# Kernel tuning notes

Hardware: AMD Instinct MI355X
Metric: run time of the kernel (lower is better)

The kernel has to match this reference:

```python
import jax, jax.numpy as jnp
import numpy as np

L_COMPUTE = 32   # topological levels after primary inputs
W = 32768        # gates per level
K = 4            # max fan-in (distinct pins 1..K per gate)
B = 128          # parallel test patterns
T = 16           # number of cell types in the library
N = (L_COMPUTE + 1) * W


def setup_inputs() -> dict:
    key = jax.random.key(0)
    k1, k2, k3, k4 = jax.random.split(key, 4)
    # binary logic values per node per pattern (only level-0 rows are real inputs;
    # the rest are overwritten by propagation, matching g.ndata['h'] = feature)
    feature = jax.random.bernoulli(k1, 0.5, (N, B)).astype(jnp.float32)
    # truth table: activation[cell_type, input_combination] in {0,1}
    activation = jax.random.bernoulli(k2, 0.5, (T, 2 ** K)).astype(jnp.float32)
    # each gate in level l draws its K inputs from level l-1
    src_idx = jax.random.randint(k3, (L_COMPUTE, W, K), 0, W).astype(jnp.int32)
    cell_type = jax.random.randint(k4, (L_COMPUTE, W), 0, T).astype(jnp.int32)
    # edge pin numbers: distinct pins 1..K per gate (edges.data['x'])
    pins = jnp.broadcast_to(jnp.arange(1, K + 1, dtype=jnp.int32), (L_COMPUTE, W, K))
    pins = jnp.asarray(pins)
    return {"feature": feature, "activation": activation, "src_idx": src_idx,
            "cell_type": cell_type, "pins": pins}


def reference(feature, activation, src_idx, cell_type, pins):
    Wn = src_idx.shape[1]
    Bn = feature.shape[1]
    h0 = feature[:Wn]  # primary-input level keeps its feature values

    def step(h, xs):
        src, ctype, pin = xs          # [W,K], [W], [W,K]
        hs = h[src]                   # gather: [W,K,B]
        # gcn_msg: m = 2^(x-1) * h_src ; gcn_reduce: sum over incoming edges
        w = jnp.exp2(pin.astype(h.dtype) - 1.0)          # [W,K]
        m = jnp.einsum('wk,wkb->wb', w, hs)              # [W,B] encoded input combo
        # NodeApplyModule: truth-table lookup activation[cell_type, h]
        h_new = activation[ctype[:, None], m.astype(jnp.int32)]  # [W,B]
        return h_new, h_new

    _, ys = jax.lax.scan(step, h0, (src_idx, cell_type, pins))
    # g.ndata.pop('h'): values for ALL nodes, level 0 unchanged
    return jnp.concatenate([h0, ys.reshape(-1, Bn)], axis=0)
```

## Files before the change

kernel.cpp:

```cpp
#include <hip/hip_runtime.h>
#include <stdint.h>

typedef uint32_t u32;
typedef unsigned long long u64;
typedef float f4 __attribute__((ext_vector_type(4)));

#define WGATES 32768
#define BATCH  128
#define LAYERS 32
#define NTYPES 16
#define NC 512
#define WPL (WGATES * 4)
#define F4L (WGATES * BATCH / 4)

#define WS_SUB_OFF    1024
#define WS_LVL2_OFF   34816
#define WS_DONE_OFF   35840
#define WS_S_OFF      69632
#define WS_NEED_BYTES ((size_t)(WS_S_OFF + 33 * WPL) * 4)

__device__ __forceinline__ u32 agent_load(const u32* p) {
    return __hip_atomic_load(p, __ATOMIC_RELAXED, __HIP_MEMORY_SCOPE_AGENT);
}
__device__ __forceinline__ void agent_store(u32* p, u32 v) {
    __hip_atomic_store(p, v, __ATOMIC_RELAXED, __HIP_MEMORY_SCOPE_AGENT);
}
__device__ __forceinline__ u32 agent_add(u32* p, u32 v) {
    return __hip_atomic_fetch_add(p, v, __ATOMIC_RELAXED, __HIP_MEMORY_SCOPE_AGENT);
}

__device__ __forceinline__ u32 lut_eval(u32 tt, u32 a, u32 b, u32 c, u32 d) {
    u32 m[16];
    #pragma unroll
    for (int j = 0; j < 16; ++j)
        m[j] = (u32)(((int)(tt << (31 - j))) >> 31);
    u32 na = ~a, nb = ~b, nc = ~c, nd = ~d;
    u32 v0 = (m[1]&a)|(m[0]&na),  v1 = (m[3]&a)|(m[2]&na);
    u32 v2 = (m[5]&a)|(m[4]&na),  v3 = (m[7]&a)|(m[6]&na);
    u32 v4 = (m[9]&a)|(m[8]&na),  v5 = (m[11]&a)|(m[10]&na);
    u32 v6 = (m[13]&a)|(m[12]&na),v7 = (m[15]&a)|(m[14]&na);
    u32 u0 = (b&v1)|(nb&v0), u1 = (b&v3)|(nb&v2);
    u32 u2 = (b&v5)|(nb&v4), u3 = (b&v7)|(nb&v6);
    u32 w0 = (c&u1)|(nc&u0), w1 = (c&u3)|(nc&u2);
    return (d&w1)|(nd&w0);
}

__device__ __forceinline__ void wait_done(const u32* ws, int l, int line, int tid) {
    if (tid == 0) {
        const u32* p = ws + WS_DONE_OFF + (size_t)l * 1024 + line * 16;
        while (agent_load(p) == 0)
            __builtin_amdgcn_s_sleep(4);
    }
    __syncthreads();
    asm volatile("" ::: "memory");
}

__global__ void pack_main(const float* __restrict__ feature,
                          const float* __restrict__ activation,
                          u32* __restrict__ ws) {
    int t = blockIdx.x * 256 + threadIdx.x;
    if (blockIdx.x == 0 && threadIdx.x < NTYPES) {
        u32 tt = 0;
        #pragma unroll
        for (int m = 0; m < 16; ++m)
            tt |= (activation[threadIdx.x * 16 + m] != 0.0f ? 1u : 0u) << m;
        ws[threadIdx.x] = tt;
    }
    int z = (int)blockIdx.x - 1;
    if (z >= 0 && z < 268)
        ws[1024 + z * 256 + threadIdx.x] = 0;
    float v = feature[t];
    u64 m = __ballot(v != 0.0f);
    if ((t & 63) == 0)
        ((u64*)(ws + WS_S_OFF))[t >> 6] = m;
}

__global__ __launch_bounds__(256) void coop_kernel(
        const int* __restrict__ src_idx,
        const int* __restrict__ cell_type,
        u32* __restrict__ ws,
        float* __restrict__ out,
        int NU)
{
    u32* Sb = ws + WS_S_OFF;
    int tid = threadIdx.x;
    __shared__ u32 stt[NTYPES];
    if (tid < NTYPES) stt[tid] = ws[tid];
    __syncthreads();

    if ((int)blockIdx.x < NC) {
        int gid = blockIdx.x * 256 + tid;
        int g = gid >> 2, q = gid & 3;
        int sub = blockIdx.x & 63;
        for (int l = 1; l <= LAYERS; ++l) {
            const int4 s = ((const int4*)(src_idx + (size_t)(l - 1) * WGATES * 4))[g];
            u32 ttv = stt[cell_type[(size_t)(l - 1) * WGATES + g]];
            if (l > 1) wait_done(ws, l - 1, sub, tid);
            const u32* Sp = Sb + (size_t)(l - 1) * WPL;
            u32 a = Sp[(u32)s.x * 4 + q];
            u32 b = Sp[(u32)s.y * 4 + q];
            u32 c = Sp[(u32)s.z * 4 + q];
            u32 d = Sp[(u32)s.w * 4 + q];
            agent_store(Sb + (size_t)l * WPL + gid, lut_eval(ttv, a, b, c, d));
            asm volatile("s_waitcnt vmcnt(0)" ::: "memory");
            __syncthreads();
            if (tid == 0) {
                u32* subp = ws + WS_SUB_OFF + (size_t)l * 1024 + sub * 16;
                u32 old = agent_add(subp, 1u);
                if (old == (u32)(NC / 64 - 1)) {
                    u32 old2 = agent_add(ws + WS_LVL2_OFF + (size_t)l * 16, 1u);
                    if (old2 == 63u) {
                        u32* donep = ws + WS_DONE_OFF + (size_t)l * 1024;
                        #pragma unroll
                        for (int j = 0; j < 64; ++j)
                            agent_store(donep + j * 16, 1u);
                    }
                }
            }
        }
    } else {
        int ub = blockIdx.x - NC;
        for (int l = 0; l <= LAYERS; ++l) {
            if (l >= 1) wait_done(ws, l, ub & 63, tid);
            const u32* Sl = Sb + (size_t)l * WPL;
            f4* ob = (f4*)(out + (size_t)l * WGATES * BATCH);
            for (u32 i = (u32)ub * 256u + tid; i < (u32)F4L; i += (u32)NU * 256u) {
                u32 wb = Sl[i >> 3];
                u32 sh = (i & 7) * 4;
                f4 f;
                f.x = ((wb >> (sh    )) & 1) ? 1.0f : 0.0f;
                f.y = ((wb >> (sh + 1)) & 1) ? 1.0f : 0.0f;
                f.z = ((wb >> (sh + 2)) & 1) ? 1.0f : 0.0f;
                f.w = ((wb >> (sh + 3)) & 1) ? 1.0f : 0.0f;
                __builtin_nontemporal_store(f, ob + i);
            }
        }
    }
}

__global__ void pack_kernel_fb(const float* __restrict__ feature,
                               const float* __restrict__ activation,
                               float* __restrict__ out,
                               u32* __restrict__ tt_ws,
                               u32* __restrict__ buf0) {
    int t = blockIdx.x * 256 + threadIdx.x;
    if (blockIdx.x == 0 && threadIdx.x < NTYPES) {
        u32 tt = 0;
        #pragma unroll
        for (int m = 0; m < 16; ++m)
            tt |= (activation[threadIdx.x * 16 + m] != 0.0f ? 1u : 0u) << m;
        tt_ws[threadIdx.x] = tt;
    }
    float v = feature[t];
    out[t] = v;
    u64 m = __ballot(v != 0.0f);
    if ((t & 63) == 0)
        ((u64*)buf0)[t >> 6] = m;
}

__global__ void fused_kernel_fb(const u32* __restrict__ prev,
                                u32* __restrict__ next,
                                const int* __restrict__ src_idx,
                                const int* __restrict__ cell_type,
                                const u32* __restrict__ tt_ws,
                                const u32* __restrict__ upacked,
                                float* __restrict__ uout,
                                int do_compute)
{
    int tid = threadIdx.x;
    if (do_compute && blockIdx.x < 512) {
        int gl = tid >> 2, q = tid & 3;
        int wg = blockIdx.x * 64 + gl;
        const int4 s = ((const int4*)src_idx)[wg];
        u32 tt = tt_ws[cell_type[wg]];
        u32 a = prev[(size_t)s.x * 4 + q];
        u32 b = prev[(size_t)s.y * 4 + q];
        u32 c = prev[(size_t)s.z * 4 + q];
        u32 d = prev[(size_t)s.w * 4 + q];
        next[(size_t)wg * 4 + q] = lut_eval(tt, a, b, c, d);
        return;
    }
    if (uout == nullptr) return;
    int ub = do_compute ? (int)blockIdx.x - 512 : (int)blockIdx.x;
    #pragma unroll
    for (int r = 0; r < 2; ++r) {
        int fi = ((ub * 2 + r) * 256 + tid) * 4;
        u32 wb = upacked[fi >> 5];
        int sh = fi & 31;
        f4 f;
        f.x = ((wb >> (sh    )) & 1) ? 1.0f : 0.0f;
        f.y = ((wb >> (sh + 1)) & 1) ? 1.0f : 0.0f;
        f.z = ((wb >> (sh + 2)) & 1) ? 1.0f : 0.0f;
        f.w = ((wb >> (sh + 3)) & 1) ? 1.0f : 0.0f;
        ((f4*)uout)[fi >> 2] = f;
    }
}

static void launch_fallback(const float* feature, const float* activation,
                            const int* src_idx, const int* cell_type,
                            float* out, void* d_ws, hipStream_t stream) {
    u32* tt_ws = (u32*)d_ws;
    u32* bufA = (u32*)((char*)d_ws + 1024);
    u32* bufB = (u32*)((char*)d_ws + 1024 + WGATES * 16);
    pack_kernel_fb<<<WGATES * BATCH / 256, 256, 0, stream>>>(
        feature, activation, out, tt_ws, bufA);
    for (int l = 1; l <= LAYERS; ++l) {
        u32* prev = ((l - 1) & 1) ? bufB : bufA;
        u32* next = ((l - 1) & 1) ? bufA : bufB;
        float* uout = (l >= 2) ? out + (size_t)(l - 1) * WGATES * BATCH : nullptr;
        fused_kernel_fb<<<512 + 2048, 256, 0, stream>>>(
            prev, next,
            src_idx + (size_t)(l - 1) * WGATES * 4,
            cell_type + (size_t)(l - 1) * WGATES,
            tt_ws, prev, uout, 1);
    }
    u32* s32 = ((LAYERS - 1) & 1) ? bufA : bufB;
    fused_kernel_fb<<<2048, 256, 0, stream>>>(
        s32, s32, src_idx, cell_type, tt_ws,
        s32, out + (size_t)LAYERS * WGATES * BATCH, 0);
}

extern "C" void kernel_launch(void* const* d_in, const int* in_sizes, int n_in,
                              void* d_out, int out_size, void* d_ws, size_t ws_size,
                              hipStream_t stream) {
    const float* feature    = (const float*)d_in[0];
    const float* activation = (const float*)d_in[1];
    const int*   src_idx    = (const int*)d_in[2];
    const int*   cell_type  = (const int*)d_in[3];
    float* out = (float*)d_out;

    bool coop_ok = (ws_size >= WS_NEED_BYTES);
    int G = 0, NU = 0;
    if (coop_ok) {
        int dev = 0;
        (void)hipGetDevice(&dev);
        int numCU = 0, bpc = 0;
        if (hipDeviceGetAttribute(&numCU, hipDeviceAttributeMultiprocessorCount, dev)
                != hipSuccess) coop_ok = false;
        if (coop_ok &&
            hipOccupancyMaxActiveBlocksPerMultiprocessor(
                &bpc, (const void*)coop_kernel, 256, 0) != hipSuccess) coop_ok = false;
        if (coop_ok) {
            G = bpc * numCU;
            if (G > 2048) G = 2048;
            NU = G - NC;
            if (NU < 256) coop_ok = false;
        }
    }

    if (coop_ok) {
        u32* ws = (u32*)d_ws;
        pack_main<<<WGATES * BATCH / 256, 256, 0, stream>>>(feature, activation, ws);
        void* args[] = {(void*)&src_idx, (void*)&cell_type, (void*)&ws,
                        (void*)&out, (void*)&NU};
        hipError_t e = hipLaunchCooperativeKernel(
            (const void*)coop_kernel, dim3(G), dim3(256), args, 0, stream);
        if (e == hipSuccess) return;
    }
    launch_fallback(feature, activation, src_idx, cell_type, out, d_ws, stream);
}
```

Baseline: 168.2 us.

## Use one thread per gate with uint4 gathers and fewer compute blocks

The compute role of the cooperative kernel now uses 128 blocks instead of 512, with one thread per gate instead of four. Each thread gathers all 128 pattern bits of every input with one 16-byte load, builds the truth-table masks once, and runs four mux evaluations. The barrier tree shrinks to 16 sub-groups, and compute waiters spin with a shorter sleep than unpack waiters. Unpack blocks are split into eight contiguous slices of each level for better locality. The aim is to cut per-level synchronisation and gather instruction counts, at the cost of less parallelism on the critical path and freeing CUs for the unpack/store work.

```diff
diff --git a/kernel.cpp b/kernel.cpp
--- a/kernel.cpp
+++ b/kernel.cpp
@@ -9,7 +9,7 @@
 #define BATCH  128
 #define LAYERS 32
 #define NTYPES 16
-#define NC 512
+#define NC 128
 #define WPL (WGATES * 4)
 #define F4L (WGATES * BATCH / 4)
 
@@ -25,15 +25,19 @@
 __device__ __forceinline__ void agent_store(u32* p, u32 v) {
     __hip_atomic_store(p, v, __ATOMIC_RELAXED, __HIP_MEMORY_SCOPE_AGENT);
 }
+__device__ __forceinline__ void agent_store64(u64* p, u64 v) {
+    __hip_atomic_store(p, v, __ATOMIC_RELAXED, __HIP_MEMORY_SCOPE_AGENT);
+}
 __device__ __forceinline__ u32 agent_add(u32* p, u32 v) {
     return __hip_atomic_fetch_add(p, v, __ATOMIC_RELAXED, __HIP_MEMORY_SCOPE_AGENT);
 }
 
-__device__ __forceinline__ u32 lut_eval(u32 tt, u32 a, u32 b, u32 c, u32 d) {
-    u32 m[16];
+__device__ __forceinline__ void lut_masks(u32 tt, u32 m[16]) {
     #pragma unroll
     for (int j = 0; j < 16; ++j)
         m[j] = (u32)(((int)(tt << (31 - j))) >> 31);
+}
+__device__ __forceinline__ u32 lut_mux(const u32 m[16], u32 a, u32 b, u32 c, u32 d) {
     u32 na = ~a, nb = ~b, nc = ~c, nd = ~d;
     u32 v0 = (m[1]&a)|(m[0]&na),  v1 = (m[3]&a)|(m[2]&na);
     u32 v2 = (m[5]&a)|(m[4]&na),  v3 = (m[7]&a)|(m[6]&na);
@@ -45,11 +49,12 @@
     return (d&w1)|(nd&w0);
 }
 
-__device__ __forceinline__ void wait_done(const u32* ws, int l, int line, int tid) {
+__device__ __forceinline__ void wait_done(const u32* ws, int l, int line,
+                                          int tid, int slp) {
     if (tid == 0) {
         const u32* p = ws + WS_DONE_OFF + (size_t)l * 1024 + line * 16;
-        while (agent_load(p) == 0)
-            __builtin_amdgcn_s_sleep(4);
+        if (slp == 1) { while (agent_load(p) == 0) __builtin_amdgcn_s_sleep(1); }
+        else         { while (agent_load(p) == 0) __builtin_amdgcn_s_sleep(8); }
     }
     __syncthreads();
     asm volatile("" ::: "memory");
@@ -89,27 +94,34 @@
     __syncthreads();
 
     if ((int)blockIdx.x < NC) {
-        int gid = blockIdx.x * 256 + tid;
-        int g = gid >> 2, q = gid & 3;
-        int sub = blockIdx.x & 63;
+        int g = blockIdx.x * 256 + tid;
+        int sub = blockIdx.x & 15;
         for (int l = 1; l <= LAYERS; ++l) {
             const int4 s = ((const int4*)(src_idx + (size_t)(l - 1) * WGATES * 4))[g];
             u32 ttv = stt[cell_type[(size_t)(l - 1) * WGATES + g]];
-            if (l > 1) wait_done(ws, l - 1, sub, tid);
-            const u32* Sp = Sb + (size_t)(l - 1) * WPL;
-            u32 a = Sp[(u32)s.x * 4 + q];
-            u32 b = Sp[(u32)s.y * 4 + q];
-            u32 c = Sp[(u32)s.z * 4 + q];
-            u32 d = Sp[(u32)s.w * 4 + q];
-            agent_store(Sb + (size_t)l * WPL + gid, lut_eval(ttv, a, b, c, d));
+            if (l > 1) wait_done(ws, l - 1, sub, tid, 1);
+            const uint4* Sp = (const uint4*)(Sb + (size_t)(l - 1) * WPL);
+            uint4 A = Sp[(u32)s.x];
+            uint4 B = Sp[(u32)s.y];
+            uint4 C = Sp[(u32)s.z];
+            uint4 D = Sp[(u32)s.w];
+            u32 m[16];
+            lut_masks(ttv, m);
+            u32 r0 = lut_mux(m, A.x, B.x, C.x, D.x);
+            u32 r1 = lut_mux(m, A.y, B.y, C.y, D.y);
+            u32 r2 = lut_mux(m, A.z, B.z, C.z, D.z);
+            u32 r3 = lut_mux(m, A.w, B.w, C.w, D.w);
+            u64* dst = (u64*)(Sb + (size_t)l * WPL + (size_t)g * 4);
+            agent_store64(dst,     ((u64)r1 << 32) | r0);
+            agent_store64(dst + 1, ((u64)r3 << 32) | r2);
             asm volatile("s_waitcnt vmcnt(0)" ::: "memory");
             __syncthreads();
             if (tid == 0) {
                 u32* subp = ws + WS_SUB_OFF + (size_t)l * 1024 + sub * 16;
                 u32 old = agent_add(subp, 1u);
-                if (old == (u32)(NC / 64 - 1)) {
+                if (old == (u32)(NC / 16 - 1)) {
                     u32 old2 = agent_add(ws + WS_LVL2_OFF + (size_t)l * 16, 1u);
-                    if (old2 == 63u) {
+                    if (old2 == 15u) {
                         u32* donep = ws + WS_DONE_OFF + (size_t)l * 1024;
                         #pragma unroll
                         for (int j = 0; j < 64; ++j)
@@ -120,19 +132,38 @@
         }
     } else {
         int ub = blockIdx.x - NC;
+        bool sliced = (NU & 7) == 0;
+        int x = ub & 7;
+        u32 per = (u32)(NU >> 3);
         for (int l = 0; l <= LAYERS; ++l) {
-            if (l >= 1) wait_done(ws, l, ub & 63, tid);
+            if (l >= 1) wait_done(ws, l, ub & 63, tid, 8);
             const u32* Sl = Sb + (size_t)l * WPL;
             f4* ob = (f4*)(out + (size_t)l * WGATES * BATCH);
-            for (u32 i = (u32)ub * 256u + tid; i < (u32)F4L; i += (u32)NU * 256u) {
-                u32 wb = Sl[i >> 3];
-                u32 sh = (i & 7) * 4;
-                f4 f;
-                f.x = ((wb >> (sh    )) & 1) ? 1.0f : 0.0f;
-                f.y = ((wb >> (sh + 1)) & 1) ? 1.0f : 0.0f;
-                f.z = ((wb >> (sh + 2)) & 1) ? 1.0f : 0.0f;
-                f.w = ((wb >> (sh + 3)) & 1) ? 1.0f : 0.0f;
-                __builtin_nontemporal_store(f, ob + i);
+            if (sliced) {
+                u32 sbeg = (u32)x * (F4L / 8), send = sbeg + F4L / 8;
+                for (u32 i = sbeg + (u32)(ub >> 3) * 256u + tid; i < send;
+                     i += per * 256u) {
+                    u32 wb = Sl[i >> 3];
+                    u32 sh = (i & 7) * 4;
+                    f4 f;
+                    f.x = ((wb >> (sh    )) & 1) ? 1.0f : 0.0f;
+                    f.y = ((wb >> (sh + 1)) & 1) ? 1.0f : 0.0f;
+                    f.z = ((wb >> (sh + 2)) & 1) ? 1.0f : 0.0f;
+                    f.w = ((wb >> (sh + 3)) & 1) ? 1.0f : 0.0f;
+                    __builtin_nontemporal_store(f, ob + i);
+                }
+            } else {
+                for (u32 i = (u32)ub * 256u + tid; i < (u32)F4L;
+                     i += (u32)NU * 256u) {
+                    u32 wb = Sl[i >> 3];
+                    u32 sh = (i & 7) * 4;
+                    f4 f;
+                    f.x = ((wb >> (sh    )) & 1) ? 1.0f : 0.0f;
+                    f.y = ((wb >> (sh + 1)) & 1) ? 1.0f : 0.0f;
+                    f.z = ((wb >> (sh + 2)) & 1) ? 1.0f : 0.0f;
+                    f.w = ((wb >> (sh + 3)) & 1) ? 1.0f : 0.0f;
+                    __builtin_nontemporal_store(f, ob + i);
+                }
             }
         }
     }
@@ -173,11 +204,13 @@
         int wg = blockIdx.x * 64 + gl;
         const int4 s = ((const int4*)src_idx)[wg];
         u32 tt = tt_ws[cell_type[wg]];
+        u32 m[16];
+        lut_masks(tt, m);
         u32 a = prev[(size_t)s.x * 4 + q];
         u32 b = prev[(size_t)s.y * 4 + q];
         u32 c = prev[(size_t)s.z * 4 + q];
         u32 d = prev[(size_t)s.w * 4 + q];
-        next[(size_t)wg * 4 + q] = lut_eval(tt, a, b, c, d);
+        next[(size_t)wg * 4 + q] = lut_mux(m, a, b, c, d);
         return;
     }
     if (uout == nullptr) return;
```

Result: no change. 166.6 us (-1.0%).

## Fuse unpack into compute blocks, drop separate unpacker blocks in cooperative kernel

Applied to the files above, without the earlier changes.

Replaces the split producer/unpacker cooperative grid with 512 symmetric blocks. Each block computes its gates for a level, stages the packed results in shared memory, and expands them straight to float output, so nothing has to re-read the packed level from global memory. The barrier tree and poll sleep are adjusted to match, and packed stores become 64-bit. The risk is that the output writes now sit on the critical path between level barriers, using only 512 blocks where the old layout used idle CUs to overlap them.

```diff
diff --git a/kernel.cpp b/kernel.cpp
--- a/kernel.cpp
+++ b/kernel.cpp
@@ -9,7 +9,7 @@
 #define BATCH  128
 #define LAYERS 32
 #define NTYPES 16
-#define NC 512
+#define NCB 512
 #define WPL (WGATES * 4)
 #define F4L (WGATES * BATCH / 4)
 
@@ -25,15 +25,19 @@
 __device__ __forceinline__ void agent_store(u32* p, u32 v) {
     __hip_atomic_store(p, v, __ATOMIC_RELAXED, __HIP_MEMORY_SCOPE_AGENT);
 }
+__device__ __forceinline__ void agent_store64(u64* p, u64 v) {
+    __hip_atomic_store(p, v, __ATOMIC_RELAXED, __HIP_MEMORY_SCOPE_AGENT);
+}
 __device__ __forceinline__ u32 agent_add(u32* p, u32 v) {
     return __hip_atomic_fetch_add(p, v, __ATOMIC_RELAXED, __HIP_MEMORY_SCOPE_AGENT);
 }
 
-__device__ __forceinline__ u32 lut_eval(u32 tt, u32 a, u32 b, u32 c, u32 d) {
-    u32 m[16];
+__device__ __forceinline__ void lut_masks(u32 tt, u32 m[16]) {
     #pragma unroll
     for (int j = 0; j < 16; ++j)
         m[j] = (u32)(((int)(tt << (31 - j))) >> 31);
+}
+__device__ __forceinline__ u32 lut_mux(const u32 m[16], u32 a, u32 b, u32 c, u32 d) {
     u32 na = ~a, nb = ~b, nc = ~c, nd = ~d;
     u32 v0 = (m[1]&a)|(m[0]&na),  v1 = (m[3]&a)|(m[2]&na);
     u32 v2 = (m[5]&a)|(m[4]&na),  v3 = (m[7]&a)|(m[6]&na);
@@ -48,8 +52,7 @@
 __device__ __forceinline__ void wait_done(const u32* ws, int l, int line, int tid) {
     if (tid == 0) {
         const u32* p = ws + WS_DONE_OFF + (size_t)l * 1024 + line * 16;
-        while (agent_load(p) == 0)
-            __builtin_amdgcn_s_sleep(4);
+        while (agent_load(p) == 0) __builtin_amdgcn_s_sleep(1);
     }
     __syncthreads();
     asm volatile("" ::: "memory");
@@ -75,65 +78,88 @@
         ((u64*)(ws + WS_S_OFF))[t >> 6] = m;
 }
 
-__global__ __launch_bounds__(256) void coop_kernel(
+__global__ __launch_bounds__(256) void coop_sym(
         const int* __restrict__ src_idx,
         const int* __restrict__ cell_type,
         u32* __restrict__ ws,
-        float* __restrict__ out,
-        int NU)
+        float* __restrict__ out)
 {
+    __shared__ u32 stt[NTYPES];
+    __shared__ u32 lp[256];
+    int tid = threadIdx.x;
+    if (tid < NTYPES) stt[tid] = ws[tid];
     u32* Sb = ws + WS_S_OFF;
-    int tid = threadIdx.x;
-    __shared__ u32 stt[NTYPES];
-    if (tid < NTYPES) stt[tid] = ws[tid];
+    int w0 = blockIdx.x * 256;
+    int g  = (w0 + tid) >> 2;
+    int q  = tid & 3;
+    int sub   = blockIdx.x & 31;
+    int dline = blockIdx.x & 63;
     __syncthreads();
 
-    if ((int)blockIdx.x < NC) {
-        int gid = blockIdx.x * 256 + tid;
-        int g = gid >> 2, q = gid & 3;
-        int sub = blockIdx.x & 63;
-        for (int l = 1; l <= LAYERS; ++l) {
-            const int4 s = ((const int4*)(src_idx + (size_t)(l - 1) * WGATES * 4))[g];
-            u32 ttv = stt[cell_type[(size_t)(l - 1) * WGATES + g]];
-            if (l > 1) wait_done(ws, l - 1, sub, tid);
-            const u32* Sp = Sb + (size_t)(l - 1) * WPL;
-            u32 a = Sp[(u32)s.x * 4 + q];
-            u32 b = Sp[(u32)s.y * 4 + q];
-            u32 c = Sp[(u32)s.z * 4 + q];
-            u32 d = Sp[(u32)s.w * 4 + q];
-            agent_store(Sb + (size_t)l * WPL + gid, lut_eval(ttv, a, b, c, d));
-            asm volatile("s_waitcnt vmcnt(0)" ::: "memory");
-            __syncthreads();
-            if (tid == 0) {
-                u32* subp = ws + WS_SUB_OFF + (size_t)l * 1024 + sub * 16;
-                u32 old = agent_add(subp, 1u);
-                if (old == (u32)(NC / 64 - 1)) {
-                    u32 old2 = agent_add(ws + WS_LVL2_OFF + (size_t)l * 16, 1u);
-                    if (old2 == 63u) {
-                        u32* donep = ws + WS_DONE_OFF + (size_t)l * 1024;
-                        #pragma unroll
-                        for (int j = 0; j < 64; ++j)
-                            agent_store(donep + j * 16, 1u);
-                    }
+    {
+        lp[tid] = Sb[w0 + tid];
+        __syncthreads();
+        f4* ob = (f4*)out + (size_t)blockIdx.x * 2048;
+        #pragma unroll
+        for (int j = 0; j < 8; ++j) {
+            int fi = j * 1024 + tid * 4;
+            u32 wb = lp[fi >> 5];
+            int sh = fi & 31;
+            f4 f;
+            f.x = ((wb >> (sh    )) & 1) ? 1.0f : 0.0f;
+            f.y = ((wb >> (sh + 1)) & 1) ? 1.0f : 0.0f;
+            f.z = ((wb >> (sh + 2)) & 1) ? 1.0f : 0.0f;
+            f.w = ((wb >> (sh + 3)) & 1) ? 1.0f : 0.0f;
+            __builtin_nontemporal_store(f, ob + (fi >> 2));
+        }
+        __syncthreads();
+    }
+
+    for (int l = 1; l <= LAYERS; ++l) {
+        const int4 s = ((const int4*)(src_idx + (size_t)(l - 1) * WGATES * 4))[g];
+        u32 ttv = stt[cell_type[(size_t)(l - 1) * WGATES + g]];
+        if (l > 1) wait_done(ws, l - 1, dline, tid);
+        const u32* Sp = Sb + (size_t)(l - 1) * WPL;
+        u32 a = Sp[(u32)s.x * 4 + q];
+        u32 b = Sp[(u32)s.y * 4 + q];
+        u32 c = Sp[(u32)s.z * 4 + q];
+        u32 d = Sp[(u32)s.w * 4 + q];
+        u32 m[16];
+        lut_masks(ttv, m);
+        u32 r = lut_mux(m, a, b, c, d);
+        lp[tid] = r;
+        __syncthreads();
+        if (tid < 128) {
+            u64 v = ((u64)lp[2 * tid + 1] << 32) | lp[2 * tid];
+            agent_store64((u64*)(Sb + (size_t)l * WPL) +
+                          (size_t)blockIdx.x * 128 + tid, v);
+        }
+        asm volatile("s_waitcnt vmcnt(0)" ::: "memory");
+        __syncthreads();
+        if (tid == 0) {
+            u32* subp = ws + WS_SUB_OFF + (size_t)l * 1024 + sub * 16;
+            if (agent_add(subp, 1u) == 15u) {
+                if (agent_add(ws + WS_LVL2_OFF + (size_t)l * 16, 1u) == 31u) {
+                    u32* donep = ws + WS_DONE_OFF + (size_t)l * 1024;
+                    #pragma unroll
+                    for (int j = 0; j < 64; ++j)
+                        agent_store(donep + j * 16, 1u);
                 }
             }
         }
-    } else {
-        int ub = blockIdx.x - NC;
-        for (int l = 0; l <= LAYERS; ++l) {
-            if (l >= 1) wait_done(ws, l, ub & 63, tid);
-            const u32* Sl = Sb + (size_t)l * WPL;
-            f4* ob = (f4*)(out + (size_t)l * WGATES * BATCH);
-            for (u32 i = (u32)ub * 256u + tid; i < (u32)F4L; i += (u32)NU * 256u) {
-                u32 wb = Sl[i >> 3];
-                u32 sh = (i & 7) * 4;
-                f4 f;
-                f.x = ((wb >> (sh    )) & 1) ? 1.0f : 0.0f;
-                f.y = ((wb >> (sh + 1)) & 1) ? 1.0f : 0.0f;
-                f.z = ((wb >> (sh + 2)) & 1) ? 1.0f : 0.0f;
-                f.w = ((wb >> (sh + 3)) & 1) ? 1.0f : 0.0f;
-                __builtin_nontemporal_store(f, ob + i);
-            }
+        f4* ob = (f4*)(out + (size_t)l * WGATES * BATCH) +
+                 (size_t)blockIdx.x * 2048;
+        #pragma unroll
+        for (int j = 0; j < 8; ++j) {
+            int fi = j * 1024 + tid * 4;
+            u32 wb = lp[fi >> 5];
+            int sh = fi & 31;
+            f4 f;
+            f.x = ((wb >> (sh    )) & 1) ? 1.0f : 0.0f;
+            f.y = ((wb >> (sh + 1)) & 1) ? 1.0f : 0.0f;
+            f.z = ((wb >> (sh + 2)) & 1) ? 1.0f : 0.0f;
+            f.w = ((wb >> (sh + 3)) & 1) ? 1.0f : 0.0f;
+            __builtin_nontemporal_store(f, ob + (fi >> 2));
         }
     }
 }
@@ -173,11 +199,13 @@
         int wg = blockIdx.x * 64 + gl;
         const int4 s = ((const int4*)src_idx)[wg];
         u32 tt = tt_ws[cell_type[wg]];
+        u32 m[16];
+        lut_masks(tt, m);
         u32 a = prev[(size_t)s.x * 4 + q];
         u32 b = prev[(size_t)s.y * 4 + q];
         u32 c = prev[(size_t)s.z * 4 + q];
         u32 d = prev[(size_t)s.w * 4 + q];
-        next[(size_t)wg * 4 + q] = lut_eval(tt, a, b, c, d);
+        next[(size_t)wg * 4 + q] = lut_mux(m, a, b, c, d);
         return;
     }
     if (uout == nullptr) return;
@@ -230,7 +258,6 @@
     float* out = (float*)d_out;
 
     bool coop_ok = (ws_size >= WS_NEED_BYTES);
-    int G = 0, NU = 0;
     if (coop_ok) {
         int dev = 0;
         (void)hipGetDevice(&dev);
@@ -239,22 +266,16 @@
                 != hipSuccess) coop_ok = false;
         if (coop_ok &&
             hipOccupancyMaxActiveBlocksPerMultiprocessor(
-                &bpc, (const void*)coop_kernel, 256, 0) != hipSuccess) coop_ok = false;
-        if (coop_ok) {
-            G = bpc * numCU;
-            if (G > 2048) G = 2048;
-            NU = G - NC;
-            if (NU < 256) coop_ok = false;
-        }
+                &bpc, (const void*)coop_sym, 256, 0) != hipSuccess) coop_ok = false;
+        if (coop_ok && bpc * numCU < NCB) coop_ok = false;
     }
 
     if (coop_ok) {
         u32* ws = (u32*)d_ws;
         pack_main<<<WGATES * BATCH / 256, 256, 0, stream>>>(feature, activation, ws);
-        void* args[] = {(void*)&src_idx, (void*)&cell_type, (void*)&ws,
-                        (void*)&out, (void*)&NU};
+        void* args[] = {(void*)&src_idx, (void*)&cell_type, (void*)&ws, (void*)&out};
         hipError_t e = hipLaunchCooperativeKernel(
-            (const void*)coop_kernel, dim3(G), dim3(256), args, 0, stream);
+            (const void*)coop_sym, dim3(NCB), dim3(256), args, 0, stream);
         if (e == hipSuccess) return;
     }
     launch_fallback(feature, activation, src_idx, cell_type, out, d_ws, stream);
```

Measured after the change: 174.4 us. +3.7%, slower.
